# Optimization experiments

Hardware: AMD Instinct MI355X
Metric: run time of the kernel (lower is better)

The kernel has to match this reference:

```python
import jax, jax.numpy as jnp
import numpy as np

B, S, D = 16, 2048, 128


def setup_inputs() -> dict:
    k = jax.random.key(0)
    k1, k2, k3, k4 = jax.random.split(k, 4)
    query = jax.random.normal(k1, (B, S, D), dtype=jnp.float32)
    key = jax.random.normal(k2, (B, S, D), dtype=jnp.float32)
    value = jax.random.normal(k3, (B, S, D), dtype=jnp.float32)
    # per-query tensor-valued inverse scale; shift away from zero for stable division
    inv_scale_factor = jax.random.uniform(k4, (B, S, 1), dtype=jnp.float32) + 0.5
    dropout_p = jnp.float32(0.1)
    return {"query": query, "key": key, "value": value,
            "inv_scale_factor": inv_scale_factor, "dropout_p": dropout_p}


def reference(query, key, value, inv_scale_factor, dropout_p):
    # QK^T: [B, Sq, Sk]
    qk = jnp.einsum('bqd,bkd->bqk', query, key)
    # tensor-valued scale divide (broadcast [B, Sq, 1] over keys)
    scaled_qk = qk / inv_scale_factor
    softmax_qk = jax.nn.softmax(scaled_qk, axis=-1)
    # dropout with a fixed RNG key (deterministic reference)
    keep_prob = 1.0 - dropout_p
    mask = jax.random.bernoulli(jax.random.key(42), keep_prob, softmax_qk.shape)
    dropout_qk = jnp.where(mask, softmax_qk / keep_prob, jnp.float32(0.0))
    # AV: [B, Sq, Dv]
    return jnp.einsum('bqk,bkv->bqv', dropout_qk, value)
```

## Files before the change

kernel.cpp:

```cpp
#include <hip/hip_runtime.h>
#include <stdint.h>


#define B_ 16
#define S_ 2048
#define D_ 128
#define TQ 64
#define TK 64
#define NT (S_ / TK)
#define KSTR 136
#define VSTR 72
#define PSTR 40

typedef float f32x4 __attribute__((ext_vector_type(4)));
typedef _Float16 f16x8 __attribute__((ext_vector_type(8)));
typedef _Float16 f16x2 __attribute__((ext_vector_type(2)));

union F32R4 { float4 q[4]; float f[16]; };

#define DPP_ROR(x, ctrl) \
  __int_as_float(__builtin_amdgcn_update_dpp(0, __float_as_int(x), (ctrl), 0xf, 0xf, true))
__device__ __forceinline__ float row16_max(float x) {
  x = fmaxf(x, DPP_ROR(x, 0x128));
  x = fmaxf(x, DPP_ROR(x, 0x124));
  x = fmaxf(x, DPP_ROR(x, 0x122));
  x = fmaxf(x, DPP_ROR(x, 0x121));
  return x;
}
__device__ __forceinline__ float row16_sum(float x) {
  x += DPP_ROR(x, 0x128);
  x += DPP_ROR(x, 0x124);
  x += DPP_ROR(x, 0x122);
  x += DPP_ROR(x, 0x121);
  return x;
}

__device__ __forceinline__ uint2 threefry2x32_0_42(uint32_t x0, uint32_t x1) {
  const uint32_t k0 = 0u, k1 = 42u;
  const uint32_t k2 = 0x1BD11BDAu ^ k0 ^ k1;
  x0 += k0; x1 += k1;
#define TFR(r) { x0 += x1; x1 = __builtin_rotateleft32(x1, r); x1 ^= x0; }
  TFR(13) TFR(15) TFR(26) TFR(6)
  x0 += k1; x1 += k2 + 1u;
  TFR(17) TFR(29) TFR(16) TFR(24)
  x0 += k2; x1 += k0 + 2u;
  TFR(13) TFR(15) TFR(26) TFR(6)
  x0 += k0; x1 += k1 + 3u;
  TFR(17) TFR(29) TFR(16) TFR(24)
  x0 += k1; x1 += k2 + 4u;
  TFR(13) TFR(15) TFR(26) TFR(6)
  x0 += k2; x1 += k0 + 5u;
#undef TFR
  return make_uint2(x0, x1);
}

__device__ __forceinline__ uint32_t jax_bits(uint32_t j) {
  const uint2 tf = threefry2x32_0_42(0u, j);
  return tf.x ^ tf.y;
}

__global__ __launch_bounds__(512, 3)
void attn_mfma_kernel(const float* __restrict__ Q, const float* __restrict__ K,
                      const float* __restrict__ V, const float* __restrict__ ISF,
                      const float* __restrict__ DP, float* __restrict__ OUT) {
  extern __shared__ __align__(16) char smem[];
  _Float16* const sK0  = (_Float16*)smem;
  _Float16* const sK1  = (_Float16*)(smem + 17408);
  _Float16* const sVT0 = (_Float16*)(smem + 34816);
  _Float16* const sVT1 = (_Float16*)(smem + 53248);
  _Float16* const sP   = (_Float16*)(smem + 71680);
  float* const sO1 = (float*)smem;
  float* const sM1 = (float*)(smem + 32768);
  float* const sL1 = (float*)(smem + 33024);

  const int t    = threadIdx.x;
  const int lane = t & 63;
  const int l15  = lane & 15;
  const int quad = lane >> 4;
  const int w    = t >> 6;
  const int qsub = w >> 1;
  const int kph  = w & 1;
  const int b    = blockIdx.y;
  const int qb   = blockIdx.x * TQ + qsub * 16;

  const float kp = 1.0f - DP[0];
  const uint32_t TH9 = (__float_as_uint(1.0f + kp) & 0x7FFFFFu) << 9;

  float m_[4], l_[4];
  uint32_t jq[4];
  #pragma unroll
  for (int r = 0; r < 4; ++r) {
    m_[r] = -INFINITY;
    l_[r] = 0.0f;
    jq[r] = ((uint32_t)b << 22)
          + (uint32_t)(qb + quad * 4 + r) * (uint32_t)S_;
  }

  f16x8 qf[4];
  {
    const int qrow = qb + l15;
    const float qs = 1.4426950408889634f / ISF[b * S_ + qrow];
    const float* qp = Q + ((size_t)(b * S_ + qrow)) * D_;
    #pragma unroll
    for (int c = 0; c < 4; ++c) {
      const float4 a  = *(const float4*)(qp + c * 32 + quad * 8);
      const float4 d2 = *(const float4*)(qp + c * 32 + quad * 8 + 4);
      const float xs[8] = {a.x, a.y, a.z, a.w, d2.x, d2.y, d2.z, d2.w};
      f16x8 h;
      #pragma unroll
      for (int j = 0; j < 8; ++j) h[j] = (_Float16)(xs[j] * qs);
      qf[c] = h;
    }
  }

  f32x4 accO[8];
  #pragma unroll
  for (int i = 0; i < 8; ++i) accO[i] = (f32x4){0.f, 0.f, 0.f, 0.f};

  _Float16* const pwv = &sP[w * 16 * PSTR];

  const int krow = t >> 3, kcol = (t & 7) * 16;
  const int vp = t & 31, dseg = (t >> 5) * 8;

  F32R4 kreg;
  F32R4 vreg;

#define ISSUE_LOADS(KT)                                                        \
  {                                                                            \
    const float4* gk4 = (const float4*)(K +                                    \
        ((size_t)(b * S_ + (KT) * TK + krow)) * D_ + kcol);                    \
    _Pragma("unroll") for (int i = 0; i < 4; ++i) kreg.q[i] = gk4[i];          \
    const float4* gv4 = (const float4*)(V +                                    \
        ((size_t)(b * S_ + (KT) * TK + 2 * vp)) * D_ + dseg);                  \
    _Pragma("unroll") for (int i = 0; i < 2; ++i) {                            \
      vreg.q[i] = gv4[i];                                                      \
      vreg.q[i + 2] = gv4[i + 32];             \
    }                                                                          \
  }

#define CONVERT_TO(KB, VB)                                                     \
  {                                                                            \
    _Pragma("unroll") for (int g = 0; g < 2; ++g) {                            \
      f16x8 h;                                                                 \
      _Pragma("unroll") for (int j = 0; j < 8; ++j)                            \
        h[j] = (_Float16)kreg.f[g * 8 + j];                                    \
      *(f16x8*)&(KB)[krow * KSTR + kcol + g * 8] = h;                          \
    }                                                                          \
    _Pragma("unroll") for (int d = 0; d < 8; ++d) {                            \
      f16x2 h = {(_Float16)vreg.f[d], (_Float16)vreg.f[8 + d]};                \
      *(f16x2*)&(VB)[(dseg + d) * VSTR + 2 * vp] = h;                          \
    }                                                                          \
  }

  ISSUE_LOADS(0)
  CONVERT_TO(sK0, sVT0)
  ISSUE_LOADS(1)
  __syncthreads();

  for (int kt = 0; kt < NT; ++kt) {
    const int cur = kt & 1;
    _Float16* const sKc = cur ? sK1 : sK0;
    _Float16* const sVc = cur ? sVT1 : sVT0;

    f32x4 s[2];
    #pragma unroll
    for (int n = 0; n < 2; ++n) {
      f32x4 a0 = (f32x4){0.f, 0.f, 0.f, 0.f};
      #pragma unroll
      for (int c = 0; c < 4; ++c) {
        const f16x8 bh = *(const f16x8*)&sKc[(kph * 32 + n * 16 + l15) * KSTR
                                             + c * 32 + quad * 8];
        a0 = __builtin_amdgcn_mfma_f32_16x16x32_f16(qf[c], bh, a0, 0, 0, 0);
      }
      s[n] = a0;
    }

    uint32_t rb[2][4];
    #pragma unroll
    for (int n = 0; n < 2; ++n) {
      const uint32_t jcol = (uint32_t)(kt * TK + kph * 32 + n * 16 + l15);
      #pragma unroll
      for (int r = 0; r < 4; ++r)
        rb[n][r] = jax_bits(jq[r] + jcol);
    }

    float mx[4];
    int changed = 0;
    #pragma unroll
    for (int r = 0; r < 4; ++r) {
      mx[r] = row16_max(fmaxf(s[0][r], s[1][r]));
      changed |= (mx[r] > m_[r] + 8.0f);
    }
    if (__ballot(changed) != 0ull) {
      #pragma unroll
      for (int r = 0; r < 4; ++r) {
        const float mnew = fmaxf(m_[r], mx[r]);
        const float alpha = __builtin_amdgcn_exp2f(m_[r] - mnew);
        m_[r] = mnew;
        l_[r] *= alpha;
        #pragma unroll
        for (int i = 0; i < 8; ++i) accO[i][r] *= alpha;
      }
    }
    #pragma unroll
    for (int r = 0; r < 4; ++r) {
      const float p0 = __builtin_amdgcn_exp2f(s[0][r] - m_[r]);
      const float p1 = __builtin_amdgcn_exp2f(s[1][r] - m_[r]);
      s[0][r] = p0;
      s[1][r] = p1;
      l_[r] += p0 + p1;
    }

    #pragma unroll
    for (int n = 0; n < 2; ++n) {
      const int col = n * 16 + l15;
      #pragma unroll
      for (int r = 0; r < 4; ++r) {
        const float pf = (rb[n][r] < TH9) ? s[n][r] : 0.0f;
        pwv[(quad * 4 + r) * PSTR + col] = (_Float16)pf;
      }
    }
    __threadfence_block();

    {
      const f16x8 ap = *(const f16x8*)&pwv[l15 * PSTR + quad * 8];
      #pragma unroll
      for (int d8 = 0; d8 < 8; ++d8) {
        const f16x8 bv = *(const f16x8*)&sVc[(d8 * 16 + l15) * VSTR
                                             + kph * 32 + quad * 8];
        accO[d8] = __builtin_amdgcn_mfma_f32_16x16x32_f16(ap, bv, accO[d8], 0, 0, 0);
      }
    }

    if (kt + 1 < NT) {
      _Float16* const sKn = cur ? sK0 : sK1;
      _Float16* const sVn = cur ? sVT0 : sVT1;
      CONVERT_TO(sKn, sVn)
      if (kt + 2 < NT) ISSUE_LOADS(kt + 2)
    }
    __syncthreads();
  }
#undef ISSUE_LOADS
#undef CONVERT_TO

  #pragma unroll
  for (int r = 0; r < 4; ++r)
    l_[r] = row16_sum(l_[r]);

  if (kph == 1) {
    if (l15 == 0) {
      #pragma unroll
      for (int r = 0; r < 4; ++r) {
        const int gr = qsub * 16 + quad * 4 + r;
        sM1[gr] = m_[r];
        sL1[gr] = l_[r];
      }
    }
    #pragma unroll
    for (int d8 = 0; d8 < 8; ++d8)
      #pragma unroll
      for (int r = 0; r < 4; ++r) {
        const int gr = qsub * 16 + quad * 4 + r;
        sO1[gr * D_ + d8 * 16 + l15] = accO[d8][r];
      }
  }
  __syncthreads();
  if (kph == 0) {
    float a0s[4], a1s[4];
    #pragma unroll
    for (int r = 0; r < 4; ++r) {
      const int gr = qsub * 16 + quad * 4 + r;
      const float m1  = sM1[gr];
      const float l1v = sL1[gr];
      const float mf = fmaxf(m_[r], m1);
      const float a0 = __builtin_amdgcn_exp2f(m_[r] - mf);
      const float a1 = __builtin_amdgcn_exp2f(m1 - mf);
      const float inv = 1.0f / ((a0 * l_[r] + a1 * l1v) * kp);
      a0s[r] = a0 * inv;
      a1s[r] = a1 * inv;
    }
    #pragma unroll
    for (int d8 = 0; d8 < 8; ++d8)
      #pragma unroll
      for (int r = 0; r < 4; ++r) {
        const int gr = qsub * 16 + quad * 4 + r;
        const float o1 = sO1[gr * D_ + d8 * 16 + l15];
        OUT[((size_t)(b * S_ + blockIdx.x * TQ + gr)) * D_ + d8 * 16 + l15] =
            accO[d8][r] * a0s[r] + o1 * a1s[r];
      }
  }
}

extern "C" void kernel_launch(void* const* d_in, const int* in_sizes, int n_in,
                              void* d_out, int out_size, void* d_ws, size_t ws_size,
                              hipStream_t stream) {
  const float* q   = (const float*)d_in[0];
  const float* k   = (const float*)d_in[1];
  const float* v   = (const float*)d_in[2];
  const float* isf = (const float*)d_in[3];
  const float* dp  = (const float*)d_in[4];
  float* out = (float*)d_out;

  dim3 grid(S_ / TQ, B_);
  attn_mfma_kernel<<<grid, dim3(512), 81920, stream>>>(q, k, v, isf, dp, out);
}
```

Before: 329.8 us.

## Pre-convert K/V to fp16 in workspace and stage V via direct global-to-LDS loads

Adds two prep kernels that convert K to fp16 and V to a transposed, padded fp16 tile layout in the workspace. The main kernel then reads K fragments straight from global memory into registers and copies V tiles into LDS with global_load_lds, with no in-kernel conversion. This removes the repeated fp32 loads and conversions, since each K/V tile was previously converted once per query block. It also cuts LDS use so that more blocks can be resident per CU. The cost is two extra launches, extra workspace traffic, and K reads that now skip LDS sharing.

Result: no change. 333.0 us (+1.0%).

```diff
diff --git a/kernel.cpp b/kernel.cpp
--- a/kernel.cpp
+++ b/kernel.cpp
@@ -8,15 +8,14 @@
 #define TQ 64
 #define TK 64
 #define NT (S_ / TK)
-#define KSTR 136
 #define VSTR 72
 #define PSTR 40
+#define VTILE (D_ * VSTR)
+#define KST_ELEMS ((size_t)B_ * S_ * D_)
 
 typedef float f32x4 __attribute__((ext_vector_type(4)));
 typedef _Float16 f16x8 __attribute__((ext_vector_type(8)));
-typedef _Float16 f16x2 __attribute__((ext_vector_type(2)));
-
-union F32R4 { float4 q[4]; float f[16]; };
+typedef _Float16 f16x4 __attribute__((ext_vector_type(4)));
 
 #define DPP_ROR(x, ctrl) \
   __int_as_float(__builtin_amdgcn_update_dpp(0, __float_as_int(x), (ctrl), 0xf, 0xf, true))
@@ -59,16 +58,48 @@
   return tf.x ^ tf.y;
 }
 
-__global__ __launch_bounds__(512, 3)
-void attn_mfma_kernel(const float* __restrict__ Q, const float* __restrict__ K,
-                      const float* __restrict__ V, const float* __restrict__ ISF,
+__global__ __launch_bounds__(256)
+void prep_k(const float* __restrict__ K, _Float16* __restrict__ Kst) {
+  const size_t i = ((size_t)blockIdx.x * 256 + threadIdx.x) * 4;
+  const float4 x = *(const float4*)(K + i);
+  f16x4 h = {(_Float16)x.x, (_Float16)x.y, (_Float16)x.z, (_Float16)x.w};
+  *(f16x4*)(Kst + i) = h;
+}
+
+__global__ __launch_bounds__(256)
+void prep_v(const float* __restrict__ V, _Float16* __restrict__ Vst) {
+  __shared__ _Float16 sT[64 * 132];
+  const int b = blockIdx.y, kt = blockIdx.x, t = threadIdx.x;
+  const int key = t >> 2, dq = t & 3;
+  const float* vp = V + ((size_t)(b * S_ + kt * 64 + key)) * D_ + dq * 32;
+  #pragma unroll
+  for (int i = 0; i < 8; ++i) {
+    const float4 x = *(const float4*)(vp + i * 4);
+    _Float16* d = &sT[key * 132 + dq * 32 + i * 4];
+    d[0] = (_Float16)x.x; d[1] = (_Float16)x.y;
+    d[2] = (_Float16)x.z; d[3] = (_Float16)x.w;
+  }
+  __syncthreads();
+  _Float16* tile = Vst + (size_t)(b * NT + kt) * VTILE;
+  #pragma unroll
+  for (int it = 0; it < 4; ++it) {
+    const int idx = t * 4 + it;
+    const int d = idx >> 3, kg = idx & 7;
+    f16x8 v;
+    #pragma unroll
+    for (int j = 0; j < 8; ++j) v[j] = sT[(kg * 8 + j) * 132 + d];
+    *(f16x8*)&tile[d * VSTR + kg * 8] = v;
+  }
+}
+
+__global__ __launch_bounds__(512, 4)
+void attn_mfma_kernel(const float* __restrict__ Q, const _Float16* __restrict__ Kst,
+                      const _Float16* __restrict__ Vst, const float* __restrict__ ISF,
                       const float* __restrict__ DP, float* __restrict__ OUT) {
-  extern __shared__ __align__(16) char smem[];
-  _Float16* const sK0  = (_Float16*)smem;
-  _Float16* const sK1  = (_Float16*)(smem + 17408);
-  _Float16* const sVT0 = (_Float16*)(smem + 34816);
-  _Float16* const sVT1 = (_Float16*)(smem + 53248);
-  _Float16* const sP   = (_Float16*)(smem + 71680);
+  __shared__ __align__(16) char smem[47104];
+  char* const sVT0 = smem;
+  char* const sVT1 = smem + 18432;
+  _Float16* const sP = (_Float16*)(smem + 36864);
   float* const sO1 = (float*)smem;
   float* const sM1 = (float*)(smem + 32768);
   float* const sL1 = (float*)(smem + 33024);
@@ -119,60 +150,44 @@
 
   _Float16* const pwv = &sP[w * 16 * PSTR];
 
-  const int krow = t >> 3, kcol = (t & 7) * 16;
-  const int vp = t & 31, dseg = (t >> 5) * 8;
-
-  F32R4 kreg;
-  F32R4 vreg;
-
-#define ISSUE_LOADS(KT)                                                        \
+#define STAGE_V(VT, SV)                                                        \
   {                                                                            \
-    const float4* gk4 = (const float4*)(K +                                    \
-        ((size_t)(b * S_ + (KT) * TK + krow)) * D_ + kcol);                    \
-    _Pragma("unroll") for (int i = 0; i < 4; ++i) kreg.q[i] = gk4[i];          \
-    const float4* gv4 = (const float4*)(V +                                    \
-        ((size_t)(b * S_ + (KT) * TK + 2 * vp)) * D_ + dseg);                  \
-    _Pragma("unroll") for (int i = 0; i < 2; ++i) {                            \
-      vreg.q[i] = gv4[i];                                                      \
-      vreg.q[i + 2] = gv4[i + 32];             \
+    const char* vsrc = (const char*)(Vst + (size_t)(b * NT + (VT)) * VTILE);   \
+    for (int s8 = w; s8 < 18; s8 += 8) {                                       \
+      __builtin_amdgcn_global_load_lds(                                        \
+          (const unsigned int*)(vsrc + s8 * 1024 + lane * 16),                 \
+          (unsigned int*)((SV) + s8 * 1024), 16, 0, 0);                        \
     }                                                                          \
   }
 
-#define CONVERT_TO(KB, VB)                                                     \
-  {                                                                            \
-    _Pragma("unroll") for (int g = 0; g < 2; ++g) {                            \
-      f16x8 h;                                                                 \
-      _Pragma("unroll") for (int j = 0; j < 8; ++j)                            \
-        h[j] = (_Float16)kreg.f[g * 8 + j];                                    \
-      *(f16x8*)&(KB)[krow * KSTR + kcol + g * 8] = h;                          \
-    }                                                                          \
-    _Pragma("unroll") for (int d = 0; d < 8; ++d) {                            \
-      f16x2 h = {(_Float16)vreg.f[d], (_Float16)vreg.f[8 + d]};                \
-      *(f16x2*)&(VB)[(dseg + d) * VSTR + 2 * vp] = h;                          \
-    }                                                                          \
-  }
-
-  ISSUE_LOADS(0)
-  CONVERT_TO(sK0, sVT0)
-  ISSUE_LOADS(1)
+  STAGE_V(0, sVT0)
   __syncthreads();
 
   for (int kt = 0; kt < NT; ++kt) {
     const int cur = kt & 1;
-    _Float16* const sKc = cur ? sK1 : sK0;
-    _Float16* const sVc = cur ? sVT1 : sVT0;
+    char* const sVc = cur ? sVT1 : sVT0;
+
+    const _Float16* kb = Kst + ((size_t)(b * S_ + kt * TK + kph * 32)) * D_;
+    f16x8 kf[2][4];
+    #pragma unroll
+    for (int n = 0; n < 2; ++n)
+      #pragma unroll
+      for (int c = 0; c < 4; ++c)
+        kf[n][c] = *(const f16x8*)(kb + (n * 16 + l15) * D_ + c * 32 + quad * 8);
 
     f32x4 s[2];
     #pragma unroll
     for (int n = 0; n < 2; ++n) {
       f32x4 a0 = (f32x4){0.f, 0.f, 0.f, 0.f};
       #pragma unroll
-      for (int c = 0; c < 4; ++c) {
-        const f16x8 bh = *(const f16x8*)&sKc[(kph * 32 + n * 16 + l15) * KSTR
-                                             + c * 32 + quad * 8];
-        a0 = __builtin_amdgcn_mfma_f32_16x16x32_f16(qf[c], bh, a0, 0, 0, 0);
-      }
+      for (int c = 0; c < 4; ++c)
+        a0 = __builtin_amdgcn_mfma_f32_16x16x32_f16(qf[c], kf[n][c], a0, 0, 0, 0);
       s[n] = a0;
+    }
+
+    if (kt + 1 < NT) {
+      char* const sVn = cur ? sVT0 : sVT1;
+      STAGE_V(kt + 1, sVn)
     }
 
     uint32_t rb[2][4];
@@ -224,24 +239,18 @@
 
     {
       const f16x8 ap = *(const f16x8*)&pwv[l15 * PSTR + quad * 8];
+      const _Float16* vb = (const _Float16*)sVc;
       #pragma unroll
       for (int d8 = 0; d8 < 8; ++d8) {
-        const f16x8 bv = *(const f16x8*)&sVc[(d8 * 16 + l15) * VSTR
-                                             + kph * 32 + quad * 8];
+        const f16x8 bv = *(const f16x8*)&vb[(d8 * 16 + l15) * VSTR
+                                            + kph * 32 + quad * 8];
         accO[d8] = __builtin_amdgcn_mfma_f32_16x16x32_f16(ap, bv, accO[d8], 0, 0, 0);
       }
     }
 
-    if (kt + 1 < NT) {
-      _Float16* const sKn = cur ? sK0 : sK1;
-      _Float16* const sVn = cur ? sVT0 : sVT1;
-      CONVERT_TO(sKn, sVn)
-      if (kt + 2 < NT) ISSUE_LOADS(kt + 2)
-    }
     __syncthreads();
   }
-#undef ISSUE_LOADS
-#undef CONVERT_TO
+#undef STAGE_V
 
   #pragma unroll
   for (int r = 0; r < 4; ++r)
@@ -301,6 +310,12 @@
   const float* dp  = (const float*)d_in[4];
   float* out = (float*)d_out;
 
+  _Float16* kst = (_Float16*)d_ws;
+  _Float16* vst = kst + KST_ELEMS;
+
+  prep_k<<<dim3(4096), dim3(256), 0, stream>>>(k, kst);
+  prep_v<<<dim3(NT, B_), dim3(256), 0, stream>>>(v, vst);
+
   dim3 grid(S_ / TQ, B_);
-  attn_mfma_kernel<<<grid, dim3(512), 81920, stream>>>(q, k, v, isf, dp, out);
-}
+  attn_mfma_kernel<<<grid, dim3(512), 0, stream>>>(q, kst, vst, isf, dp, out);
+}
```
